# Optimization experiments

Measured on AMD Instinct MI355X. Metric: run time of the kernel, lower is better.

Reference implementation:

```python
import jax, jax.numpy as jnp
import numpy as np

B, P, M, CI, CO, W = 8, 16384, 16, 16, 32, 17
RES_RATE = 0.5
SQ_CONV = float(np.sqrt(1.0 - RES_RATE))
SQ_RES = float(np.sqrt(RES_RATE))


def setup_inputs() -> dict:
    key = jax.random.key(0)
    k0, k1, k2, k3, k4 = jax.random.split(key, 5)
    in_pc = jax.random.normal(k0, (B, P, CI), dtype=jnp.float32)
    # neighbor ids in [0, P]; value P is the padding sentinel (masked out)
    neighbor_id = jax.random.randint(k1, (P, M), 0, P + 1)
    weights = jax.random.normal(k2, (W, CO * CI), dtype=jnp.float32)
    bias = jnp.zeros((P, CO), dtype=jnp.float32)  # perpoint_bias == 1
    w_weights = jax.random.normal(k3, (P, M, W), dtype=jnp.float32) / (M * W)
    weight_res = jax.random.normal(k4, (CO, CI), dtype=jnp.float32) / CO
    return {
        "in_pc": in_pc,
        "weights": weights,
        "bias": bias,
        "w_weights": w_weights,
        "weight_res": weight_res,
        "neighbor_id": neighbor_id,
    }


def reference(in_pc, weights, bias, w_weights, weight_res, neighbor_id):
    b = in_pc.shape[0]
    # mask: 1 for real neighbor, 0 for padding sentinel (id == P)
    mask = (neighbor_id != P).astype(in_pc.dtype)  # [P, M]
    # pad point cloud with one zero point so sentinel index gathers zeros
    in_pc_pad = jnp.concatenate(
        [in_pc, jnp.zeros((b, 1, CI), dtype=in_pc.dtype)], axis=1
    )  # [B, P+1, CI]
    in_neighbors = in_pc_pad[:, neighbor_id]  # [B, P, M, CI]
    # per-point conv weights: masked learned combination of basis weights
    ww = w_weights * mask[:, :, None]  # [P, M, W]
    Wpm = jnp.einsum("pmw,wc->pmc", ww, weights).reshape(P, M, CO, CI)
    # gather-generate-matmul: contract neighbors with per-point weights, sum over M
    out_pc_conv = jnp.einsum("pmoi,bpmi->bpo", Wpm, in_neighbors) + bias
    out_pc_conv = jax.nn.elu(out_pc_conv)  # not final layer
    # residual branch: channel projection (in_c != out_c), identity over points
    out_pc_res = jnp.einsum("oi,bpi->bpo", weight_res, in_pc_pad)[:, :P]
    return out_pc_conv * SQ_CONV + out_pc_res * SQ_RES
```

## Files before the change

### kernel.cpp

```cpp
#include <hip/hip_runtime.h>

#define PP 16384
#define SQH 0.70710678118654752440f

typedef unsigned int u32;
typedef unsigned short u16;
typedef __attribute__((ext_vector_type(8))) short bfrag;
typedef __attribute__((ext_vector_type(4))) float ffrag;
typedef __attribute__((ext_vector_type(16))) float ffrag16;
typedef __attribute__((ext_vector_type(4))) float f4;
typedef __attribute__((ext_vector_type(2))) float f2;

union BU { bfrag v; uint4 u; };

__device__ __forceinline__ u32 pk2(float a, float b) {
  u32 ua = __float_as_uint(a), ub = __float_as_uint(b);
  return ((ua + 0x8000u) >> 16) | ((ub + 0x8000u) & 0xffff0000u);
}

#define XTB_U16 ((PP + 1) * 128)
#define XTB_B   (XTB_U16 * 2)
#define WW1_B   (XTB_B)
#define WB_B    (XTB_B + PP * 1024)
#define WR_B    (WB_B + 18432)
#define XDW     ((PP + 1) * 64)
#define NW1     (PP * 64)

__global__ void prep_kernel(const float* __restrict__ in_pc,
                            const float* __restrict__ weights,
                            const float* __restrict__ w_weights,
                            const float* __restrict__ weight_res,
                            u32* __restrict__ ws) {
  int gid = blockIdx.x * 256 + threadIdx.x;
  if (gid < XDW) {
    int p = gid >> 6, c = gid & 63;
    u32 dw = 0u;
    if (p < PP) {
      int b = c >> 3, i0 = (c & 7) * 2;
      const float* s = in_pc + ((size_t)b * PP + p) * 16 + i0;
      dw = pk2(s[0], s[1]);
    }
    ws[gid] = dw;
    return;
  }
  int e = gid - XDW;
  if (e < NW1) {
    int p = e >> 6, l = e & 63;
    int h = l >> 5, col = l & 31;
    float v[8];
#pragma unroll
    for (int idx = 0; idx < 8; ++idx)
      v[idx] = (col < 17) ? w_weights[(size_t)p * 272 + (h * 8 + idx) * 17 + col] : 0.f;
    uint4 pkd = make_uint4(pk2(v[0], v[1]), pk2(v[2], v[3]), pk2(v[4], v[5]), pk2(v[6], v[7]));
    *(uint4*)((char*)ws + WW1_B + (size_t)e * 16) = pkd;
    return;
  }
  e -= NW1;
  if (e < 1152) {
    int nt = e / 576, rem = e - nt * 576;
    int ks = rem >> 6, l = rem & 63;
    int quad = l >> 4, n = l & 15;
    int k0 = ks * 32 + quad * 8;
    uint4 pkd = make_uint4(0u, 0u, 0u, 0u);
    if (k0 < 272) {
      int w = k0 >> 4, i0 = k0 & 15;
      const float* src = weights + w * 512 + (nt * 16 + n) * 16 + i0;
      f4 lo = *(const f4*)src;
      f4 hi = *(const f4*)(src + 4);
      pkd = make_uint4(pk2(lo.x, lo.y), pk2(lo.z, lo.w), pk2(hi.x, hi.y), pk2(hi.z, hi.w));
    }
    *(uint4*)((char*)ws + WB_B + (size_t)e * 16) = pkd;
  } else if (e < 1280) {
    int l2 = e - 1152, nt = l2 >> 6, l = l2 & 63;
    int quad = l >> 4, n = l & 15;
    uint4 pkd = make_uint4(0u, 0u, 0u, 0u);
    if (quad < 2) {
      const float* src = weight_res + (nt * 16 + n) * 16 + quad * 8;
      f4 lo = *(const f4*)src;
      f4 hi = *(const f4*)(src + 4);
      pkd = make_uint4(pk2(lo.x, lo.y), pk2(lo.z, lo.w), pk2(hi.x, hi.y), pk2(hi.z, hi.w));
    }
    *(uint4*)((char*)ws + WR_B + (size_t)(e - 1152) * 16) = pkd;
  }
}

__global__ __launch_bounds__(256, 4) void pconv_main(
    const u32* __restrict__ ws,
    const float* __restrict__ bias,
    const int*  __restrict__ nidg,
    float* __restrict__ out)
{
  __shared__ __attribute__((aligned(16))) u16 Abuf[4 * 16 * 296];

  const u16*  __restrict__ xTb = (const u16*)ws;
  const uint4* __restrict__ WW1 = (const uint4*)((const char*)ws + WW1_B);
  const uint4* __restrict__ WB  = (const uint4*)((const char*)ws + WB_B);
  const uint4* __restrict__ WR  = (const uint4*)((const char*)ws + WR_B);

  const int tid = threadIdx.x;
  const int wid = __builtin_amdgcn_readfirstlane(tid >> 6);
  const int lane = tid & 63;
  const int lo16 = lane & 15, quad = lane >> 4;
  const int col = lane & 31, h = lane >> 5;
  u16* __restrict__ Aw = Abuf + wid * (16 * 296);

  const int pair = blockIdx.x * 4 + wid;
  const int p0 = pair * 2;

  {
    int r = lane >> 2, c = lane & 3;
    *(uint2*)(Aw + r * 296 + 272 + c * 4) = make_uint2(0u, 0u);
  }

  const int* __restrict__ nid0p = nidg + p0 * 16;
  const int* __restrict__ nid1p = nidg + (p0 + 1) * 16;
  int nid0[16], nid1[16];
#pragma unroll
  for (int m = 0; m < 16; ++m) nid0[m] = nid0p[m];
#pragma unroll
  for (int m = 0; m < 16; ++m) nid1[m] = nid1p[m];

  BU bb0, bb1;
  bb0.u = WW1[(size_t)p0 * 64 + lane];
  bb1.u = WW1[(size_t)(p0 + 1) * 64 + lane];

  const int voffb = (col >> 4) * 16 + (col & 15);

  u32 a0[4][4], a1[4][4];
#pragma unroll
  for (int j = 0; j < 4; ++j) {
    const u16* q0 = xTb + (size_t)nid0[h * 8 + 2 * j] * 128 + voffb;
    const u16* q1 = xTb + (size_t)nid0[h * 8 + 2 * j + 1] * 128 + voffb;
#pragma unroll
    for (int t = 0; t < 4; ++t)
      a0[t][j] = (u32)q0[t * 32] | ((u32)q1[t * 32] << 16);
  }
#pragma unroll
  for (int j = 0; j < 4; ++j) {
    const u16* q0 = xTb + (size_t)nid1[h * 8 + 2 * j] * 128 + voffb;
    const u16* q1 = xTb + (size_t)nid1[h * 8 + 2 * j + 1] * 128 + voffb;
#pragma unroll
    for (int t = 0; t < 4; ++t)
      a1[t][j] = (u32)q0[t * 32] | ((u32)q1[t * 32] << 16);
  }

#pragma unroll
  for (int pt = 0; pt < 2; ++pt) {
    const u32 (&ad)[4][4] = pt ? a1 : a0;
    BU bb = pt ? bb1 : bb0;
#pragma unroll
    for (int t = 0; t < 4; ++t) {
      BU aa;
      aa.u = make_uint4(ad[t][0], ad[t][1], ad[t][2], ad[t][3]);
      ffrag16 c = {};
      c = __builtin_amdgcn_mfma_f32_32x32x16_bf16(aa.v, bb.v, c, 0, 0, 0);
      if (col < 17) {
#pragma unroll
        for (int q = 0; q < 4; ++q) {
          int r = pt * 8 + 2 * t + (q >> 1);
          int i0 = 4 * h + 8 * (q & 1);
          u16* dst = Aw + r * 296 + col * 16 + i0;
          *(uint2*)dst = make_uint2(pk2(c[4 * q + 0], c[4 * q + 1]),
                                    pk2(c[4 * q + 2], c[4 * q + 3]));
        }
      }
    }
  }

  ffrag acc0 = {0.f, 0.f, 0.f, 0.f}, acc1 = {0.f, 0.f, 0.f, 0.f};
#pragma unroll
  for (int ks = 0; ks < 9; ++ks) {
    bfrag af = *(const bfrag*)(Aw + lo16 * 296 + ks * 32 + quad * 8);
    BU b0, b1;
    b0.u = WB[ks * 64 + lane];
    b1.u = WB[576 + ks * 64 + lane];
    acc0 = __builtin_amdgcn_mfma_f32_16x16x32_bf16(af, b0.v, acc0, 0, 0, 0);
    acc1 = __builtin_amdgcn_mfma_f32_16x16x32_bf16(af, b1.v, acc1, 0, 0, 0);
  }
  {
    const int p_r = p0 + (lo16 >> 3), b_r = lo16 & 7;
    BU su;
    su.u = make_uint4(0u, 0u, 0u, 0u);
    if (quad < 2)
      su.u = *(const uint4*)(xTb + (size_t)p_r * 128 + b_r * 16 + quad * 8);
    BU rb0, rb1;
    rb0.u = WR[lane];
    rb1.u = WR[64 + lane];
    ffrag rz = {0.f, 0.f, 0.f, 0.f};
    ffrag res0 = __builtin_amdgcn_mfma_f32_16x16x32_bf16(su.v, rb0.v, rz, 0, 0, 0);
    ffrag res1 = __builtin_amdgcn_mfma_f32_16x16x32_bf16(su.v, rb1.v, rz, 0, 0, 0);

    float* Ef = (float*)Aw;
#pragma unroll
    for (int j = 0; j < 4; ++j) {
      int r = quad * 4 + j;
      int p_e = p0 + (r >> 3);
      float c0 = acc0[j] + bias[(size_t)p_e * 32 + lo16];
      float c1 = acc1[j] + bias[(size_t)p_e * 32 + 16 + lo16];
      float e0 = c0 > 0.f ? c0 : (__expf(c0) - 1.f);
      float e1 = c1 > 0.f ? c1 : (__expf(c1) - 1.f);
      Ef[r * 40 + lo16]      = SQH * e0 + SQH * res0[j];
      Ef[r * 40 + 16 + lo16] = SQH * e1 + SQH * res1[j];
    }
#pragma unroll
    for (int k = 0; k < 2; ++k) {
      int rr = (lane >> 3) + 8 * k;
      int cc = lane & 7;
      f4 v = *(const f4*)(Ef + rr * 40 + cc * 4);
      int p_s = p0 + (rr >> 3), b_s = rr & 7;
      *(f4*)(out + ((size_t)b_s * PP + p_s) * 32 + cc * 4) = v;
    }
  }
}

extern "C" void kernel_launch(void* const* d_in, const int* in_sizes, int n_in,
                              void* d_out, int out_size, void* d_ws, size_t ws_size,
                              hipStream_t stream) {
  const float* in_pc       = (const float*)d_in[0];
  const float* weights     = (const float*)d_in[1];
  const float* bias        = (const float*)d_in[2];
  const float* w_weights   = (const float*)d_in[3];
  const float* weight_res  = (const float*)d_in[4];
  const int*   neighbor_id = (const int*)d_in[5];
  float* out = (float*)d_out;
  u32* ws = (u32*)d_ws;

  int prep_threads = XDW + NW1 + 1280;
  hipLaunchKernelGGL(prep_kernel, dim3((prep_threads + 255) / 256), dim3(256), 0, stream,
                     in_pc, weights, w_weights, weight_res, ws);
  hipLaunchKernelGGL(pconv_main, dim3(2048), dim3(256), 0, stream,
                     ws, bias, neighbor_id, out);
}
```

Baseline: 107.4 us.

## Fuse w_weights conversion into main kernel and process four points per wave

The bf16 repacking of w_weights moves out of the prep kernel into the main kernel, which now reads the fp32 values directly. This removes a full intermediate write and re-read of a large workspace buffer. The prep kernel now transposes in_pc through LDS so its global reads and writes are coalesced. Each wave now handles four points, issuing all neighbor gathers up front and loading the residual weights once; this adds register pressure that may lower occupancy or cause spills.

```diff
diff --git a/kernel.cpp b/kernel.cpp
--- a/kernel.cpp
+++ b/kernel.cpp
@@ -9,7 +9,6 @@
 typedef __attribute__((ext_vector_type(4))) float ffrag;
 typedef __attribute__((ext_vector_type(16))) float ffrag16;
 typedef __attribute__((ext_vector_type(4))) float f4;
-typedef __attribute__((ext_vector_type(2))) float f2;
 
 union BU { bfrag v; uint4 u; };
 
@@ -18,44 +17,37 @@
   return ((ua + 0x8000u) >> 16) | ((ub + 0x8000u) & 0xffff0000u);
 }
 
-#define XTB_U16 ((PP + 1) * 128)
-#define XTB_B   (XTB_U16 * 2)
-#define WW1_B   (XTB_B)
-#define WB_B    (XTB_B + PP * 1024)
-#define WR_B    (WB_B + 18432)
-#define XDW     ((PP + 1) * 64)
-#define NW1     (PP * 64)
-
-__global__ void prep_kernel(const float* __restrict__ in_pc,
-                            const float* __restrict__ weights,
-                            const float* __restrict__ w_weights,
-                            const float* __restrict__ weight_res,
-                            u32* __restrict__ ws) {
-  int gid = blockIdx.x * 256 + threadIdx.x;
-  if (gid < XDW) {
-    int p = gid >> 6, c = gid & 63;
-    u32 dw = 0u;
-    if (p < PP) {
-      int b = c >> 3, i0 = (c & 7) * 2;
-      const float* s = in_pc + ((size_t)b * PP + p) * 16 + i0;
-      dw = pk2(s[0], s[1]);
-    }
-    ws[gid] = dw;
+#define XTB_B ((size_t)(PP + 1) * 256)
+#define WB_B  XTB_B
+#define WR_B  (XTB_B + 18432)
+
+__global__ __launch_bounds__(256) void prep_kernel(
+    const float* __restrict__ in_pc, const float* __restrict__ weights,
+    const float* __restrict__ weight_res, u32* __restrict__ ws) {
+  __shared__ u32 T[64 * 72];
+  const int blk = blockIdx.x, t = threadIdx.x;
+  if (blk < 256) {
+    const int p0 = blk * 64;
+    const int pl = t >> 2, i4 = t & 3;
+#pragma unroll
+    for (int b = 0; b < 8; ++b) {
+      f4 v = *(const f4*)(in_pc + ((size_t)b * PP + p0 + pl) * 16 + i4 * 4);
+      T[pl * 72 + b * 8 + i4 * 2]     = pk2(v.x, v.y);
+      T[pl * 72 + b * 8 + i4 * 2 + 1] = pk2(v.z, v.w);
+    }
+    __syncthreads();
+#pragma unroll
+    for (int k = 0; k < 4; ++k) {
+      int idx = k * 256 + t;
+      int pl2 = idx >> 4, c2 = (idx & 15) * 4;
+      uint4 v = *(const uint4*)&T[pl2 * 72 + c2];
+      *(uint4*)&ws[(size_t)(p0 + pl2) * 64 + c2] = v;
+    }
     return;
   }
-  int e = gid - XDW;
-  if (e < NW1) {
-    int p = e >> 6, l = e & 63;
-    int h = l >> 5, col = l & 31;
-    float v[8];
-#pragma unroll
-    for (int idx = 0; idx < 8; ++idx)
-      v[idx] = (col < 17) ? w_weights[(size_t)p * 272 + (h * 8 + idx) * 17 + col] : 0.f;
-    uint4 pkd = make_uint4(pk2(v[0], v[1]), pk2(v[2], v[3]), pk2(v[4], v[5]), pk2(v[6], v[7]));
-    *(uint4*)((char*)ws + WW1_B + (size_t)e * 16) = pkd;
-    return;
-  }
-  e -= NW1;
+  if (blk == 256 && t < 32)
+    *(uint2*)&ws[(size_t)PP * 64 + t * 2] = make_uint2(0u, 0u);
+  int e = (blk - 256) * 256 + t;
   if (e < 1152) {
     int nt = e / 576, rem = e - nt * 576;
     int ks = rem >> 6, l = rem & 63;
@@ -87,15 +79,15 @@
 __global__ __launch_bounds__(256, 4) void pconv_main(
     const u32* __restrict__ ws,
     const float* __restrict__ bias,
+    const float* __restrict__ wwg,
     const int*  __restrict__ nidg,
     float* __restrict__ out)
 {
   __shared__ __attribute__((aligned(16))) u16 Abuf[4 * 16 * 296];
 
   const u16*  __restrict__ xTb = (const u16*)ws;
-  const uint4* __restrict__ WW1 = (const uint4*)((const char*)ws + WW1_B);
-  const uint4* __restrict__ WB  = (const uint4*)((const char*)ws + WB_B);
-  const uint4* __restrict__ WR  = (const uint4*)((const char*)ws + WR_B);
+  const uint4* __restrict__ WB = (const uint4*)((const char*)ws + WB_B);
+  const uint4* __restrict__ WR = (const uint4*)((const char*)ws + WR_B);
 
   const int tid = threadIdx.x;
   const int wid = __builtin_amdgcn_readfirstlane(tid >> 6);
@@ -104,88 +96,91 @@
   const int col = lane & 31, h = lane >> 5;
   u16* __restrict__ Aw = Abuf + wid * (16 * 296);
 
-  const int pair = blockIdx.x * 4 + wid;
-  const int p0 = pair * 2;
-
-  {
-    int r = lane >> 2, c = lane & 3;
-    *(uint2*)(Aw + r * 296 + 272 + c * 4) = make_uint2(0u, 0u);
-  }
-
-  const int* __restrict__ nid0p = nidg + p0 * 16;
-  const int* __restrict__ nid1p = nidg + (p0 + 1) * 16;
-  int nid0[16], nid1[16];
-#pragma unroll
-  for (int m = 0; m < 16; ++m) nid0[m] = nid0p[m];
-#pragma unroll
-  for (int m = 0; m < 16; ++m) nid1[m] = nid1p[m];
-
-  BU bb0, bb1;
-  bb0.u = WW1[(size_t)p0 * 64 + lane];
-  bb1.u = WW1[(size_t)(p0 + 1) * 64 + lane];
+  const int p0 = (blockIdx.x * 4 + wid) * 4;
+
+  int nid[4][16];
+#pragma unroll
+  for (int pt = 0; pt < 4; ++pt)
+#pragma unroll
+    for (int m = 0; m < 16; ++m) nid[pt][m] = nidg[(size_t)(p0 + pt) * 16 + m];
+
+  BU bb[4];
+#pragma unroll
+  for (int pt = 0; pt < 4; ++pt) {
+    float v[8];
+#pragma unroll
+    for (int idx = 0; idx < 8; ++idx) {
+      float x = 0.f;
+      if (col < 17) x = wwg[(size_t)(p0 + pt) * 272 + (h * 8 + idx) * 17 + col];
+      v[idx] = x;
+    }
+    bb[pt].u = make_uint4(pk2(v[0], v[1]), pk2(v[2], v[3]), pk2(v[4], v[5]), pk2(v[6], v[7]));
+  }
 
   const int voffb = (col >> 4) * 16 + (col & 15);
-
-  u32 a0[4][4], a1[4][4];
-#pragma unroll
-  for (int j = 0; j < 4; ++j) {
-    const u16* q0 = xTb + (size_t)nid0[h * 8 + 2 * j] * 128 + voffb;
-    const u16* q1 = xTb + (size_t)nid0[h * 8 + 2 * j + 1] * 128 + voffb;
-#pragma unroll
-    for (int t = 0; t < 4; ++t)
-      a0[t][j] = (u32)q0[t * 32] | ((u32)q1[t * 32] << 16);
-  }
-#pragma unroll
-  for (int j = 0; j < 4; ++j) {
-    const u16* q0 = xTb + (size_t)nid1[h * 8 + 2 * j] * 128 + voffb;
-    const u16* q1 = xTb + (size_t)nid1[h * 8 + 2 * j + 1] * 128 + voffb;
-#pragma unroll
-    for (int t = 0; t < 4; ++t)
-      a1[t][j] = (u32)q0[t * 32] | ((u32)q1[t * 32] << 16);
-  }
-
-#pragma unroll
-  for (int pt = 0; pt < 2; ++pt) {
-    const u32 (&ad)[4][4] = pt ? a1 : a0;
-    BU bb = pt ? bb1 : bb0;
-#pragma unroll
-    for (int t = 0; t < 4; ++t) {
-      BU aa;
-      aa.u = make_uint4(ad[t][0], ad[t][1], ad[t][2], ad[t][3]);
-      ffrag16 c = {};
-      c = __builtin_amdgcn_mfma_f32_32x32x16_bf16(aa.v, bb.v, c, 0, 0, 0);
-      if (col < 17) {
-#pragma unroll
-        for (int q = 0; q < 4; ++q) {
-          int r = pt * 8 + 2 * t + (q >> 1);
-          int i0 = 4 * h + 8 * (q & 1);
-          u16* dst = Aw + r * 296 + col * 16 + i0;
-          *(uint2*)dst = make_uint2(pk2(c[4 * q + 0], c[4 * q + 1]),
-                                    pk2(c[4 * q + 2], c[4 * q + 3]));
+  u32 ag[4][16];
+#pragma unroll
+  for (int pt = 0; pt < 4; ++pt)
+#pragma unroll
+    for (int j = 0; j < 4; ++j) {
+      const u16* q0 = xTb + (size_t)nid[pt][h * 8 + 2 * j] * 128 + voffb;
+      const u16* q1 = xTb + (size_t)nid[pt][h * 8 + 2 * j + 1] * 128 + voffb;
+#pragma unroll
+      for (int t = 0; t < 4; ++t)
+        ag[pt][t * 4 + j] = (u32)q0[t * 32] | ((u32)q1[t * 32] << 16);
+    }
+
+  BU rb0, rb1;
+  rb0.u = WR[lane];
+  rb1.u = WR[64 + lane];
+
+#pragma unroll
+  for (int pair = 0; pair < 2; ++pair) {
+    const int pp0 = p0 + pair * 2;
+
+    {
+      int r = lane >> 2, c = lane & 3;
+      *(uint2*)(Aw + r * 296 + 272 + c * 4) = make_uint2(0u, 0u);
+    }
+
+#pragma unroll
+    for (int pt2 = 0; pt2 < 2; ++pt2) {
+      const int pt = pair * 2 + pt2;
+#pragma unroll
+      for (int t = 0; t < 4; ++t) {
+        BU aa;
+        aa.u = make_uint4(ag[pt][t * 4 + 0], ag[pt][t * 4 + 1],
+                          ag[pt][t * 4 + 2], ag[pt][t * 4 + 3]);
+        ffrag16 c = {};
+        c = __builtin_amdgcn_mfma_f32_32x32x16_bf16(aa.v, bb[pt].v, c, 0, 0, 0);
+        if (col < 17) {
+#pragma unroll
+          for (int q = 0; q < 4; ++q) {
+            int r = pt2 * 8 + 2 * t + (q >> 1);
+            int i0 = 4 * h + 8 * (q & 1);
+            u16* dst = Aw + r * 296 + col * 16 + i0;
+            *(uint2*)dst = make_uint2(pk2(c[4 * q + 0], c[4 * q + 1]),
+                                      pk2(c[4 * q + 2], c[4 * q + 3]));
+          }
         }
       }
     }
-  }
-
-  ffrag acc0 = {0.f, 0.f, 0.f, 0.f}, acc1 = {0.f, 0.f, 0.f, 0.f};
-#pragma unroll
-  for (int ks = 0; ks < 9; ++ks) {
-    bfrag af = *(const bfrag*)(Aw + lo16 * 296 + ks * 32 + quad * 8);
-    BU b0, b1;
-    b0.u = WB[ks * 64 + lane];
-    b1.u = WB[576 + ks * 64 + lane];
-    acc0 = __builtin_amdgcn_mfma_f32_16x16x32_bf16(af, b0.v, acc0, 0, 0, 0);
-    acc1 = __builtin_amdgcn_mfma_f32_16x16x32_bf16(af, b1.v, acc1, 0, 0, 0);
-  }
-  {
-    const int p_r = p0 + (lo16 >> 3), b_r = lo16 & 7;
+
+    ffrag acc0 = {0.f, 0.f, 0.f, 0.f}, acc1 = {0.f, 0.f, 0.f, 0.f};
+#pragma unroll
+    for (int ks = 0; ks < 9; ++ks) {
+      bfrag af = *(const bfrag*)(Aw + lo16 * 296 + ks * 32 + quad * 8);
+      BU b0, b1;
+      b0.u = WB[ks * 64 + lane];
+      b1.u = WB[576 + ks * 64 + lane];
+      acc0 = __builtin_amdgcn_mfma_f32_16x16x32_bf16(af, b0.v, acc0, 0, 0, 0);
+      acc1 = __builtin_amdgcn_mfma_f32_16x16x32_bf16(af, b1.v, acc1, 0, 0, 0);
+    }
+    const int p_r = pp0 + (lo16 >> 3), b_r = lo16 & 7;
     BU su;
     su.u = make_uint4(0u, 0u, 0u, 0u);
     if (quad < 2)
       su.u = *(const uint4*)(xTb + (size_t)p_r * 128 + b_r * 16 + quad * 8);
-    BU rb0, rb1;
-    rb0.u = WR[lane];
-    rb1.u = WR[64 + lane];
     ffrag rz = {0.f, 0.f, 0.f, 0.f};
     ffrag res0 = __builtin_amdgcn_mfma_f32_16x16x32_bf16(su.v, rb0.v, rz, 0, 0, 0);
     ffrag res1 = __builtin_amdgcn_mfma_f32_16x16x32_bf16(su.v, rb1.v, rz, 0, 0, 0);
@@ -194,7 +189,7 @@
 #pragma unroll
     for (int j = 0; j < 4; ++j) {
       int r = quad * 4 + j;
-      int p_e = p0 + (r >> 3);
+      int p_e = pp0 + (r >> 3);
       float c0 = acc0[j] + bias[(size_t)p_e * 32 + lo16];
       float c1 = acc1[j] + bias[(size_t)p_e * 32 + 16 + lo16];
       float e0 = c0 > 0.f ? c0 : (__expf(c0) - 1.f);
@@ -207,7 +202,7 @@
       int rr = (lane >> 3) + 8 * k;
       int cc = lane & 7;
       f4 v = *(const f4*)(Ef + rr * 40 + cc * 4);
-      int p_s = p0 + (rr >> 3), b_s = rr & 7;
+      int p_s = pp0 + (rr >> 3), b_s = rr & 7;
       *(f4*)(out + ((size_t)b_s * PP + p_s) * 32 + cc * 4) = v;
     }
   }
@@ -225,9 +220,8 @@
   float* out = (float*)d_out;
   u32* ws = (u32*)d_ws;
 
-  int prep_threads = XDW + NW1 + 1280;
-  hipLaunchKernelGGL(prep_kernel, dim3((prep_threads + 255) / 256), dim3(256), 0, stream,
-                     in_pc, weights, w_weights, weight_res, ws);
-  hipLaunchKernelGGL(pconv_main, dim3(2048), dim3(256), 0, stream,
-                     ws, bias, neighbor_id, out);
-}
+  hipLaunchKernelGGL(prep_kernel, dim3(261), dim3(256), 0, stream,
+                     in_pc, weights, weight_res, ws);
+  hipLaunchKernelGGL(pconv_main, dim3(1024), dim3(256), 0, stream,
+                     ws, bias, w_weights, neighbor_id, out);
+}
```

After: 151.3 us. 1.41x slower.
